# Optimization experiments

Hardware: AMD Instinct MI355X
Metric: run time of the kernel (lower is better)

The kernel has to match this reference:

```python
import jax, jax.numpy as jnp
import numpy as np

B, C, D, H, K = 512, 112, 128, 8, 8  # batch, channels(=seq), d_model, heads, conv kernel
HD = D // H
SCALE = HD ** -0.5
BN_EPS = 1e-5
LN_EPS = 1e-5


def setup_inputs() -> dict:
    key = jax.random.key(0)
    ks = jax.random.split(key, 12)
    s = 0.05
    return {
        "x": jax.random.normal(ks[0], (B, C, D), jnp.float32),
        "conv_w": jax.random.normal(ks[1], (C, 1, K), jnp.float32) * s,
        "conv_b": jax.random.normal(ks[2], (C,), jnp.float32) * s,
        "bn_g": jnp.ones((C,), jnp.float32),
        "bn_b": jnp.zeros((C,), jnp.float32),
        "bn_m": jnp.zeros((C,), jnp.float32),
        "bn_v": jnp.ones((C,), jnp.float32),
        "wq": jax.random.normal(ks[3], (D, D), jnp.float32) * s,
        "bq": jax.random.normal(ks[4], (D,), jnp.float32) * s,
        "wk": jax.random.normal(ks[5], (D, D), jnp.float32) * s,
        "bk": jax.random.normal(ks[6], (D,), jnp.float32) * s,
        "wv": jax.random.normal(ks[7], (D, D), jnp.float32) * s,
        "bv": jax.random.normal(ks[8], (D,), jnp.float32) * s,
        "wo": jax.random.normal(ks[9], (D, D), jnp.float32) * s,
        "bo": jax.random.normal(ks[10], (D,), jnp.float32) * s,
        "ln_g": jnp.ones((D,), jnp.float32),
        "ln_b": jnp.zeros((D,), jnp.float32),
    }


def _forward(x, conv_w, conv_b, bn_g, bn_b, bn_m, bn_v,
             wq, bq, wk, bk, wv, bv, wo, bo, ln_g, ln_b):
    # resnet_1: depthwise Conv1d(padding='same', k=8) -> GELU -> BatchNorm1d (eval)
    # torch 'same' padding for even k: left = (k-1)//2 = 3, right = 4
    h = jax.lax.conv_general_dilated(
        x, conv_w, window_strides=(1,), padding=[(3, 4)],
        dimension_numbers=("NCH", "OIH", "NCH"), feature_group_count=C)
    h = h + conv_b[None, :, None]
    h = jax.nn.gelu(h, approximate=False)
    h = (h - bn_m[None, :, None]) * (bn_g[None, :, None] * jax.lax.rsqrt(bn_v + BN_EPS)[None, :, None]) + bn_b[None, :, None]
    src = x + h  # [B, C, D]; attention treats C as sequence dim

    # multi-head attention (hand-rolled, res_attention path with prev=None)
    q = (src @ wq.T + bq).reshape(B, C, H, HD).transpose(0, 2, 1, 3)  # [B,H,S,hd]
    k = (src @ wk.T + bk).reshape(B, C, H, HD).transpose(0, 2, 1, 3)
    v = (src @ wv.T + bv).reshape(B, C, H, HD).transpose(0, 2, 1, 3)
    scores = jnp.einsum("bhqd,bhkd->bhqk", q, k) * SCALE  # [B,H,S,S]
    attn = jax.nn.softmax(scores, axis=-1)
    out = jnp.einsum("bhqk,bhkd->bhqd", attn, v)  # [B,H,S,hd]
    out = out.transpose(0, 2, 1, 3).reshape(B, C, D)
    out = out @ wo.T + bo

    # residual + LayerNorm over last dim
    src = src + out
    mu = jnp.mean(src, axis=-1, keepdims=True)
    var = jnp.mean(jnp.square(src - mu), axis=-1, keepdims=True)
    src = (src - mu) * jax.lax.rsqrt(var + LN_EPS) * ln_g + ln_b
    return src


def reference(x, conv_w, conv_b, bn_g, bn_b, bn_m, bn_v,
              wq, bq, wk, bk, wv, bv, wo, bo, ln_g, ln_b):
    return _forward(x, conv_w, conv_b, bn_g, bn_b, bn_m, bn_v,
                    wq, bq, wk, bk, wv, bv, wo, bo, ln_g, ln_b)
```

## Files before the change

### kernel.cpp

```cpp
#include <hip/hip_runtime.h>
#include <hip/hip_bf16.h>

#define BB 512
#define CC 112
#define DD 128
#define HH 8
#define HD 16
#define KK 8
#define SROW 140
#define QS 1792

typedef unsigned short u16;
typedef short short8 __attribute__((ext_vector_type(8)));
typedef float f32x4 __attribute__((ext_vector_type(4)));
typedef float f32x16 __attribute__((ext_vector_type(16)));

#define MFMA16(a, b, c) __builtin_amdgcn_mfma_f32_16x16x32_bf16(a, b, c, 0, 0, 0)
#define MFMA32(a, b, c) __builtin_amdgcn_mfma_f32_32x32x16_bf16(a, b, c, 0, 0, 0)

__device__ inline u16 f2bf(float f) {
  union { float f; unsigned u; } v{f};
  unsigned r = (v.u + 0x7FFFu + ((v.u >> 16) & 1u)) >> 16;
  return (u16)r;
}
__device__ inline float bf2f(u16 u) {
  union { unsigned u; float f; } v;
  v.u = ((unsigned)u) << 16;
  return v.f;
}
__device__ inline unsigned pk2(float a, float b) {
  __hip_bfloat162 h = __float22bfloat162_rn(float2{a, b});
  union { __hip_bfloat162 h; unsigned u; } v{h};
  return v.u;
}

__device__ inline unsigned permx32(unsigned x) {
  unsigned a = x, b = x;
  asm("v_permlane32_swap_b32 %0, %1" : "+v"(a), "+v"(b));
  return (threadIdx.x & 32) ? a : b;
}
__device__ inline float permx32f(float x) {
  union { float f; unsigned u; } v{x};
  v.u = permx32(v.u);
  return v.f;
}

__global__ __launch_bounds__(256) void k_wcvt(
    const float* __restrict__ wq, const float* __restrict__ wk,
    const float* __restrict__ wv, const float* __restrict__ wo,
    u16* __restrict__ w_b) {
  const int i = (blockIdx.x * 256 + threadIdx.x);
  const int sel = i >> 12, off = i & 4095;
  const float* w = (sel == 0) ? wq : (sel == 1) ? wk : (sel == 2) ? wv : wo;
  const float4 v = ((const float4*)w)[off];
  ((uint2*)w_b)[i] = uint2{pk2(v.x, v.y), pk2(v.z, v.w)};
}

__global__ __launch_bounds__(1024, 4) void k_fused(
    const float* __restrict__ x, const float* __restrict__ cw,
    const float* __restrict__ cb, const float* __restrict__ bg,
    const float* __restrict__ bb_, const float* __restrict__ bm,
    const float* __restrict__ bv, const u16* __restrict__ w_b,
    const float* __restrict__ bq, const float* __restrict__ bk,
    const float* __restrict__ bvv, const float* __restrict__ bo,
    const float* __restrict__ lg, const float* __restrict__ lb,
    float* __restrict__ out) {
  __shared__ __attribute__((aligned(16))) u16 S[CC * SROW];
  __shared__ __attribute__((aligned(16))) u16 QL[HH * CC * HD];
  __shared__ __attribute__((aligned(16))) u16 KL[HH * CC * HD];
  __shared__ __attribute__((aligned(16))) u16 VTL[HH * HD * CC];
  const int b = blockIdx.x;
  const int t = threadIdx.x;
  const int wave = t >> 6, lane = t & 63;

  const int tg = t >> 3, s = t & 7;
  if (tg < CC) {
    const int row = tg, ch = tg;
    const float4 w0 = *(const float4*)(cw + ch * KK);
    const float4 w1 = *(const float4*)(cw + ch * KK + 4);
    const float cbv = cb[ch];
    const float bscale = bg[ch] * rsqrtf(bv[ch] + 1e-5f);
    const float bmv = bm[ch], bbv = bb_[ch];
    const float* __restrict__ xr = x + ((size_t)b * CC + row) * DD;
    float in[24];
#pragma unroll
    for (int f = 0; f < 6; ++f) {
      const int fi = 4 * s - 1 + f;
      float4 vv = {0.f, 0.f, 0.f, 0.f};
      if (fi >= 0 && fi < 32) vv = ((const float4*)xr)[fi];
      in[f * 4 + 0] = vv.x; in[f * 4 + 1] = vv.y;
      in[f * 4 + 2] = vv.z; in[f * 4 + 3] = vv.w;
    }
    unsigned pkv[8];
#pragma unroll
    for (int i2 = 0; i2 < 8; ++i2) {
      float oo[2];
#pragma unroll
      for (int j = 0; j < 2; ++j) {
        const int i = i2 * 2 + j;
        float a = 0.f;
        a = fmaf(in[i + 1], w0.x, a);
        a = fmaf(in[i + 2], w0.y, a);
        a = fmaf(in[i + 3], w0.z, a);
        a = fmaf(in[i + 4], w0.w, a);
        a = fmaf(in[i + 5], w1.x, a);
        a = fmaf(in[i + 6], w1.y, a);
        a = fmaf(in[i + 7], w1.z, a);
        a = fmaf(in[i + 8], w1.w, a);
        a += cbv;
        const float u = fmaf(0.044715f * a, a, 1.0f);
        const float e = __expf(a * u * -1.5957691216f);
        const float g = a * __frcp_rn(1.f + e);
        oo[j] = in[i + 4] + (g - bmv) * bscale + bbv;
      }
      pkv[i2] = pk2(oo[0], oo[1]);
    }
    u16* srow = S + row * SROW + s * 16;
#pragma unroll
    for (int k2 = 0; k2 < 4; ++k2)
      *(uint2*)(srow + k2 * 4) = ((uint2*)pkv)[k2];
  }
  __syncthreads();

  {
    const int h = wave >> 1, mh = wave & 1;
    const int quad = lane >> 4, n = lane & 15;
    short8 Bf0[4], Bf1[4], Bf2[4];
#pragma unroll
    for (int kf = 0; kf < 4; ++kf) {
      const int wi = (h * 16 + n) * DD + kf * 32 + quad * 8;
      Bf0[kf] = *(const short8*)(w_b + wi);
      Bf1[kf] = *(const short8*)(w_b + 16384 + wi);
      Bf2[kf] = *(const short8*)(w_b + 32768 + wi);
    }
    const float bqv = bq[h * 16 + n];
    const float bkv = bk[h * 16 + n];
    const float bvv2 = bvv[h * 16 + n];
    u16* qlh = QL + h * QS;
    u16* klh = KL + h * QS;
    u16* vlh = VTL + h * QS;
#pragma unroll
    for (int m = 0; m < 4; ++m) {
      const int mt = mh * 4 + m;
      if (mt < 7) {
        short8 A[4];
#pragma unroll
        for (int kf = 0; kf < 4; ++kf)
          A[kf] = *(const short8*)&S[(mt * 16 + n) * SROW + kf * 32 + quad * 8];
        f32x4 aq = {0.f, 0.f, 0.f, 0.f};
        f32x4 ak = {0.f, 0.f, 0.f, 0.f};
        f32x4 av = {0.f, 0.f, 0.f, 0.f};
#pragma unroll
        for (int kf = 0; kf < 4; ++kf) {
          aq = MFMA16(A[kf], Bf0[kf], aq);
          ak = MFMA16(A[kf], Bf1[kf], ak);
          av = MFMA16(A[kf], Bf2[kf], av);
        }
        const int row0 = mt * 16 + quad * 4;
#pragma unroll
        for (int r = 0; r < 4; ++r) {
          qlh[(row0 + r) * HD + n] = f2bf(aq[r] + bqv);
          klh[(row0 + r) * HD + n] = f2bf(ak[r] + bkv);
        }
        *(uint2*)&vlh[n * CC + row0] =
            uint2{pk2(av[0] + bvv2, av[1] + bvv2),
                  pk2(av[2] + bvv2, av[3] + bvv2)};
      }
    }
  }
  __syncthreads();

  {
    const int h = wave >> 1, qh = wave & 1;
    const int lo = lane & 31, hi = lane >> 5, hi8 = hi * 8;
    const u16* qlh = QL + h * QS;
    const u16* klh = KL + h * QS;
    const u16* vlh = VTL + h * QS;
    u16* aoh = QL + h * QS;
    for (int qi = 0; qi < 2; ++qi) {
      const int qt = qh * 2 + qi;
      const int qt0 = qt * 32;
      short8 Bq = {};
      if (qt0 + lo < CC) Bq = *(const short8*)(qlh + (qt0 + lo) * HD + hi8);
      f32x16 sa[4];
#pragma unroll
      for (int mt = 0; mt < 4; ++mt) {
        short8 Ak = {};
        const int key = mt * 32 + lo;
        if (key < CC) Ak = *(const short8*)(klh + key * HD + hi8);
        f32x16 z = {};
        sa[mt] = MFMA32(Ak, Bq, z);
      }
      const float C1 = 0.25f * 1.44269504088896341f;
      float mxp[4] = {-1e30f, -1e30f, -1e30f, -1e30f};
#pragma unroll
      for (int mt = 0; mt < 4; ++mt) {
        const int rmax = (mt == 3) ? 8 : 16;
#pragma unroll
        for (int r = 0; r < 16; ++r)
          if (r < rmax) mxp[r & 3] = fmaxf(mxp[r & 3], sa[mt][r]);
      }
      float mx = fmaxf(fmaxf(mxp[0], mxp[1]), fmaxf(mxp[2], mxp[3]));
      mx = fmaxf(mx, permx32f(mx));
      const float mxc = mx * C1;
      float sp[4] = {0.f, 0.f, 0.f, 0.f};
#pragma unroll
      for (int mt = 0; mt < 4; ++mt) {
        const int rmax = (mt == 3) ? 8 : 16;
#pragma unroll
        for (int r = 0; r < 16; ++r)
          if (r < rmax) {
            const float p = exp2f(fmaf(sa[mt][r], C1, -mxc));
            sa[mt][r] = p;
            sp[r & 3] += p;
          }
      }
      float sum = (sp[0] + sp[1]) + (sp[2] + sp[3]);
      sum += permx32f(sum);
      const float rinv = 1.f / sum;
      unsigned U0[4][4], U1[4][4];
#pragma unroll
      for (int mt = 0; mt < 4; ++mt) {
        const int rqmax = (mt == 3) ? 2 : 4;
#pragma unroll
        for (int rq = 0; rq < 4; ++rq)
          if (rq < rqmax) {
            U0[mt][rq] =
                pk2(sa[mt][4 * rq + 0] * rinv, sa[mt][4 * rq + 1] * rinv);
            U1[mt][rq] =
                pk2(sa[mt][4 * rq + 2] * rinv, sa[mt][4 * rq + 3] * rinv);
          }
      }
      f32x16 oacc = {};
#pragma unroll
      for (int kt = 0; kt < 7; ++kt) {
        const int mt = kt >> 1;
        const int c = 2 * (kt & 1);
        const unsigned own0 = hi ? U0[mt][c + 1] : U0[mt][c];
        const unsigned own1 = hi ? U1[mt][c + 1] : U1[mt][c];
        const unsigned snd0 = hi ? U0[mt][c] : U0[mt][c + 1];
        const unsigned snd1 = hi ? U1[mt][c] : U1[mt][c + 1];
        const unsigned got0 = permx32(snd0);
        const unsigned got1 = permx32(snd1);
        union { unsigned u[4]; short8 s; } ap;
        ap.u[0] = hi ? got0 : own0;
        ap.u[1] = hi ? got1 : own1;
        ap.u[2] = hi ? own0 : got0;
        ap.u[3] = hi ? own1 : got1;
        short8 Bv = {};
        if (lo < HD) Bv = *(const short8*)(vlh + lo * CC + kt * 16 + hi8);
        oacc = MFMA32(ap.s, Bv, oacc);
      }
      if (lo < HD) {
#pragma unroll
        for (int r = 0; r < 16; ++r) {
          const int rr = (r & 3) + 8 * (r >> 2) + 4 * hi;
          if (qt0 + rr < CC) aoh[(qt0 + rr) * HD + lo] = f2bf(oacc[r]);
        }
      }
    }
  }
  __syncthreads();

  if (wave < 7) {
    const int quad = lane >> 4, n = lane & 15;
    const int mt = wave;
    const u16* __restrict__ w_bo = w_b + 3 * 16384;
    short8 A[4];
#pragma unroll
    for (int kf = 0; kf < 4; ++kf) {
      const int head = 2 * kf + (quad >> 1);
      A[kf] = *(const short8*)&QL[head * QS + (mt * 16 + n) * HD + (quad & 1) * 8];
    }
    float v[8][4];
#pragma unroll
    for (int nt = 0; nt < 8; ++nt) {
      f32x4 acc = {0.f, 0.f, 0.f, 0.f};
#pragma unroll
      for (int kf = 0; kf < 4; ++kf) {
        const short8 Bf =
            *(const short8*)(w_bo + (nt * 16 + n) * DD + kf * 32 + quad * 8);
        acc = MFMA16(A[kf], Bf, acc);
      }
      const int col = nt * 16 + n;
      const float bcol = bo[col];
#pragma unroll
      for (int r = 0; r < 4; ++r)
        v[nt][r] = acc[r] + bcol +
                   bf2f(S[(mt * 16 + quad * 4 + r) * SROW + col]);
    }
    float sum[4] = {0.f, 0.f, 0.f, 0.f}, sq[4] = {0.f, 0.f, 0.f, 0.f};
#pragma unroll
    for (int nt = 0; nt < 8; ++nt)
#pragma unroll
      for (int r = 0; r < 4; ++r) {
        sum[r] += v[nt][r];
        sq[r] = fmaf(v[nt][r], v[nt][r], sq[r]);
      }
#pragma unroll
    for (int d = 1; d < 16; d <<= 1)
#pragma unroll
      for (int r = 0; r < 4; ++r) {
        sum[r] += __shfl_xor(sum[r], d);
        sq[r] += __shfl_xor(sq[r], d);
      }
    float mu[4], rs[4];
#pragma unroll
    for (int r = 0; r < 4; ++r) {
      mu[r] = sum[r] * (1.f / DD);
      const float var = sq[r] * (1.f / DD) - mu[r] * mu[r];
      rs[r] = rsqrtf(var + 1e-5f);
    }
#pragma unroll
    for (int nt = 0; nt < 8; ++nt) {
      const int col = nt * 16 + n;
      const float g = lg[col], be = lb[col];
#pragma unroll
      for (int r = 0; r < 4; ++r)
        out[((size_t)b * CC + mt * 16 + quad * 4 + r) * DD + col] =
            (v[nt][r] - mu[r]) * rs[r] * g + be;
    }
  }
}

extern "C" void kernel_launch(void* const* d_in, const int* in_sizes, int n_in,
                              void* d_out, int out_size, void* d_ws,
                              size_t ws_size, hipStream_t stream) {
  (void)in_sizes; (void)n_in; (void)out_size; (void)ws_size;
  const float* x   = (const float*)d_in[0];
  const float* cw  = (const float*)d_in[1];
  const float* cb  = (const float*)d_in[2];
  const float* bg  = (const float*)d_in[3];
  const float* bb  = (const float*)d_in[4];
  const float* bm  = (const float*)d_in[5];
  const float* bv  = (const float*)d_in[6];
  const float* wq  = (const float*)d_in[7];
  const float* bq  = (const float*)d_in[8];
  const float* wk  = (const float*)d_in[9];
  const float* bk  = (const float*)d_in[10];
  const float* wv  = (const float*)d_in[11];
  const float* bvv = (const float*)d_in[12];
  const float* wo  = (const float*)d_in[13];
  const float* bo  = (const float*)d_in[14];
  const float* lg  = (const float*)d_in[15];
  const float* lb  = (const float*)d_in[16];
  float* out = (float*)d_out;

  u16* w_b = (u16*)d_ws;

  k_wcvt<<<64, 256, 0, stream>>>(wq, wk, wv, wo, w_b);
  k_fused<<<BB, 1024, 0, stream>>>(x, cw, cb, bg, bb, bm, bv, w_b, bq, bk,
                                   bvv, bo, lg, lb, out);
}
```

Before: 173.3 us.

## Split fused kernel into conv and attention kernels with register-resident V

```diff
diff --git a/kernel.cpp b/kernel.cpp
--- a/kernel.cpp
+++ b/kernel.cpp
@@ -7,7 +7,6 @@
 #define HH 8
 #define HD 16
 #define KK 8
-#define SROW 140
 #define QS 1792
 
 typedef unsigned short u16;
@@ -45,35 +44,17 @@
   return v.f;
 }
 
-__global__ __launch_bounds__(256) void k_wcvt(
-    const float* __restrict__ wq, const float* __restrict__ wk,
-    const float* __restrict__ wv, const float* __restrict__ wo,
-    u16* __restrict__ w_b) {
-  const int i = (blockIdx.x * 256 + threadIdx.x);
-  const int sel = i >> 12, off = i & 4095;
-  const float* w = (sel == 0) ? wq : (sel == 1) ? wk : (sel == 2) ? wv : wo;
-  const float4 v = ((const float4*)w)[off];
-  ((uint2*)w_b)[i] = uint2{pk2(v.x, v.y), pk2(v.z, v.w)};
-}
-
-__global__ __launch_bounds__(1024, 4) void k_fused(
+__global__ __launch_bounds__(512, 4) void k_conv(
     const float* __restrict__ x, const float* __restrict__ cw,
     const float* __restrict__ cb, const float* __restrict__ bg,
     const float* __restrict__ bb_, const float* __restrict__ bm,
-    const float* __restrict__ bv, const u16* __restrict__ w_b,
-    const float* __restrict__ bq, const float* __restrict__ bk,
-    const float* __restrict__ bvv, const float* __restrict__ bo,
-    const float* __restrict__ lg, const float* __restrict__ lb,
-    float* __restrict__ out) {
-  __shared__ __attribute__((aligned(16))) u16 S[CC * SROW];
-  __shared__ __attribute__((aligned(16))) u16 QL[HH * CC * HD];
-  __shared__ __attribute__((aligned(16))) u16 KL[HH * CC * HD];
-  __shared__ __attribute__((aligned(16))) u16 VTL[HH * HD * CC];
+    const float* __restrict__ bv, const float* __restrict__ wq,
+    const float* __restrict__ wk, const float* __restrict__ wv,
+    const float* __restrict__ wo, u16* __restrict__ src_b,
+    u16* __restrict__ w_b) {
   const int b = blockIdx.x;
   const int t = threadIdx.x;
-  const int wave = t >> 6, lane = t & 63;
-
-  const int tg = t >> 3, s = t & 7;
+  const int tg = t >> 2, sub = t & 3;
   if (tg < CC) {
     const int row = tg, ch = tg;
     const float4 w0 = *(const float4*)(cw + ch * KK);
@@ -82,18 +63,18 @@
     const float bscale = bg[ch] * rsqrtf(bv[ch] + 1e-5f);
     const float bmv = bm[ch], bbv = bb_[ch];
     const float* __restrict__ xr = x + ((size_t)b * CC + row) * DD;
-    float in[24];
-#pragma unroll
-    for (int f = 0; f < 6; ++f) {
-      const int fi = 4 * s - 1 + f;
+    float in[40];
+#pragma unroll
+    for (int f = 0; f < 10; ++f) {
+      const int fi = 8 * sub - 1 + f;
       float4 vv = {0.f, 0.f, 0.f, 0.f};
       if (fi >= 0 && fi < 32) vv = ((const float4*)xr)[fi];
       in[f * 4 + 0] = vv.x; in[f * 4 + 1] = vv.y;
       in[f * 4 + 2] = vv.z; in[f * 4 + 3] = vv.w;
     }
-    unsigned pkv[8];
-#pragma unroll
-    for (int i2 = 0; i2 < 8; ++i2) {
+    unsigned pkv[16];
+#pragma unroll
+    for (int i2 = 0; i2 < 16; ++i2) {
       float oo[2];
 #pragma unroll
       for (int j = 0; j < 2; ++j) {
@@ -110,78 +91,87 @@
         a += cbv;
         const float u = fmaf(0.044715f * a, a, 1.0f);
         const float e = __expf(a * u * -1.5957691216f);
-        const float g = a * __frcp_rn(1.f + e);
-        oo[j] = in[i + 4] + (g - bmv) * bscale + bbv;
+        const float g2 = a * __frcp_rn(1.f + e);
+        oo[j] = in[i + 4] + (g2 - bmv) * bscale + bbv;
       }
       pkv[i2] = pk2(oo[0], oo[1]);
     }
-    u16* srow = S + row * SROW + s * 16;
-#pragma unroll
-    for (int k2 = 0; k2 < 4; ++k2)
-      *(uint2*)(srow + k2 * 4) = ((uint2*)pkv)[k2];
+    uint4* gsr = (uint4*)(src_b + ((size_t)b * CC + row) * DD + sub * 32);
+#pragma unroll
+    for (int k4 = 0; k4 < 4; ++k4) gsr[k4] = ((uint4*)pkv)[k4];
+  } else if (t >= 448) {
+    const int p = b * 64 + (t - 448);
+    const int sel = p >> 13, off = p & 8191;
+    const float* w = (sel == 0) ? wq : (sel == 1) ? wk : (sel == 2) ? wv : wo;
+    const float2 v = ((const float2*)w)[off];
+    ((unsigned*)w_b)[p] = pk2(v.x, v.y);
   }
-  __syncthreads();
-
+}
+
+__global__ __launch_bounds__(512, 4) void k_main(
+    const u16* __restrict__ src_b, const u16* __restrict__ w_b,
+    const float* __restrict__ bq, const float* __restrict__ bk,
+    const float* __restrict__ bvv, const float* __restrict__ bo,
+    const float* __restrict__ lg, const float* __restrict__ lb,
+    float* __restrict__ out) {
+  __shared__ __attribute__((aligned(16))) u16 QO[HH * CC * HD];
+  __shared__ __attribute__((aligned(16))) u16 KL[HH * CC * HD];
+  const int b = blockIdx.x;
+  const int t = threadIdx.x;
+  const int wave = t >> 6, lane = t & 63;
+  const int h = wave;
+  const int quad = lane >> 4, n = lane & 15;
+
+  unsigned pv[14];
   {
-    const int h = wave >> 1, mh = wave & 1;
-    const int quad = lane >> 4, n = lane & 15;
-    short8 Bf0[4], Bf1[4], Bf2[4];
+    short8 Wq[4], Wk[4], Wv[4];
 #pragma unroll
     for (int kf = 0; kf < 4; ++kf) {
       const int wi = (h * 16 + n) * DD + kf * 32 + quad * 8;
-      Bf0[kf] = *(const short8*)(w_b + wi);
-      Bf1[kf] = *(const short8*)(w_b + 16384 + wi);
-      Bf2[kf] = *(const short8*)(w_b + 32768 + wi);
+      Wq[kf] = *(const short8*)(w_b + wi);
+      Wk[kf] = *(const short8*)(w_b + 16384 + wi);
+      Wv[kf] = *(const short8*)(w_b + 32768 + wi);
     }
     const float bqv = bq[h * 16 + n];
     const float bkv = bk[h * 16 + n];
     const float bvv2 = bvv[h * 16 + n];
-    u16* qlh = QL + h * QS;
+    u16* qoh = QO + h * QS;
     u16* klh = KL + h * QS;
-    u16* vlh = VTL + h * QS;
-#pragma unroll
-    for (int m = 0; m < 4; ++m) {
-      const int mt = mh * 4 + m;
-      if (mt < 7) {
-        short8 A[4];
-#pragma unroll
-        for (int kf = 0; kf < 4; ++kf)
-          A[kf] = *(const short8*)&S[(mt * 16 + n) * SROW + kf * 32 + quad * 8];
-        f32x4 aq = {0.f, 0.f, 0.f, 0.f};
-        f32x4 ak = {0.f, 0.f, 0.f, 0.f};
-        f32x4 av = {0.f, 0.f, 0.f, 0.f};
-#pragma unroll
-        for (int kf = 0; kf < 4; ++kf) {
-          aq = MFMA16(A[kf], Bf0[kf], aq);
-          ak = MFMA16(A[kf], Bf1[kf], ak);
-          av = MFMA16(A[kf], Bf2[kf], av);
-        }
-        const int row0 = mt * 16 + quad * 4;
-#pragma unroll
-        for (int r = 0; r < 4; ++r) {
-          qlh[(row0 + r) * HD + n] = f2bf(aq[r] + bqv);
-          klh[(row0 + r) * HD + n] = f2bf(ak[r] + bkv);
-        }
-        *(uint2*)&vlh[n * CC + row0] =
-            uint2{pk2(av[0] + bvv2, av[1] + bvv2),
-                  pk2(av[2] + bvv2, av[3] + bvv2)};
-      }
+    const u16* __restrict__ sp = src_b + (size_t)b * CC * DD;
+#pragma unroll
+    for (int mt = 0; mt < 7; ++mt) {
+      short8 A[4];
+#pragma unroll
+      for (int kf = 0; kf < 4; ++kf)
+        A[kf] = *(const short8*)(sp + (mt * 16 + n) * DD + kf * 32 + quad * 8);
+      f32x4 aq = {0.f, 0.f, 0.f, 0.f};
+      f32x4 ak = {0.f, 0.f, 0.f, 0.f};
+      f32x4 av = {0.f, 0.f, 0.f, 0.f};
+#pragma unroll
+      for (int kf = 0; kf < 4; ++kf) {
+        aq = MFMA16(A[kf], Wq[kf], aq);
+        ak = MFMA16(A[kf], Wk[kf], ak);
+        av = MFMA16(A[kf], Wv[kf], av);
+      }
+      const int row0 = mt * 16 + quad * 4;
+#pragma unroll
+      for (int r = 0; r < 4; ++r) {
+        qoh[(row0 + r) * HD + n] = f2bf(aq[r] + bqv);
+        klh[(row0 + r) * HD + n] = f2bf(ak[r] + bkv);
+      }
+      pv[2 * mt] = pk2(av[0] + bvv2, av[1] + bvv2);
+      pv[2 * mt + 1] = pk2(av[2] + bvv2, av[3] + bvv2);
     }
   }
-  __syncthreads();
 
   {
-    const int h = wave >> 1, qh = wave & 1;
     const int lo = lane & 31, hi = lane >> 5, hi8 = hi * 8;
-    const u16* qlh = QL + h * QS;
+    u16* qoh = QO + h * QS;
     const u16* klh = KL + h * QS;
-    const u16* vlh = VTL + h * QS;
-    u16* aoh = QL + h * QS;
-    for (int qi = 0; qi < 2; ++qi) {
-      const int qt = qh * 2 + qi;
+    for (int qt = 0; qt < 4; ++qt) {
       const int qt0 = qt * 32;
       short8 Bq = {};
-      if (qt0 + lo < CC) Bq = *(const short8*)(qlh + (qt0 + lo) * HD + hi8);
+      if (qt0 + lo < CC) Bq = *(const short8*)(qoh + (qt0 + lo) * HD + hi8);
       f32x16 sa[4];
 #pragma unroll
       for (int mt = 0; mt < 4; ++mt) {
@@ -203,7 +193,7 @@
       float mx = fmaxf(fmaxf(mxp[0], mxp[1]), fmaxf(mxp[2], mxp[3]));
       mx = fmaxf(mx, permx32f(mx));
       const float mxc = mx * C1;
-      float sp[4] = {0.f, 0.f, 0.f, 0.f};
+      float sp4[4] = {0.f, 0.f, 0.f, 0.f};
 #pragma unroll
       for (int mt = 0; mt < 4; ++mt) {
         const int rmax = (mt == 3) ? 8 : 16;
@@ -212,10 +202,10 @@
           if (r < rmax) {
             const float p = exp2f(fmaf(sa[mt][r], C1, -mxc));
             sa[mt][r] = p;
-            sp[r & 3] += p;
+            sp4[r & 3] += p;
           }
       }
-      float sum = (sp[0] + sp[1]) + (sp[2] + sp[3]);
+      float sum = (sp4[0] + sp4[1]) + (sp4[2] + sp4[3]);
       sum += permx32f(sum);
       const float rinv = 1.f / sum;
       unsigned U0[4][4], U1[4][4];
@@ -247,15 +237,18 @@
         ap.u[1] = hi ? got1 : own1;
         ap.u[2] = hi ? own0 : got0;
         ap.u[3] = hi ? own1 : got1;
-        short8 Bv = {};
-        if (lo < HD) Bv = *(const short8*)(vlh + lo * CC + kt * 16 + hi8);
-        oacc = MFMA32(ap.s, Bv, oacc);
+        union { unsigned u[4]; short8 s; } bvf;
+        bvf.u[0] = pv[2 * kt];
+        bvf.u[1] = pv[2 * kt + 1];
+        bvf.u[2] = __shfl_xor(pv[2 * kt], 16);
+        bvf.u[3] = __shfl_xor(pv[2 * kt + 1], 16);
+        oacc = MFMA32(ap.s, bvf.s, oacc);
       }
       if (lo < HD) {
 #pragma unroll
         for (int r = 0; r < 16; ++r) {
           const int rr = (r & 3) + 8 * (r >> 2) + 4 * hi;
-          if (qt0 + rr < CC) aoh[(qt0 + rr) * HD + lo] = f2bf(oacc[r]);
+          if (qt0 + rr < CC) qoh[(qt0 + rr) * HD + lo] = f2bf(oacc[r]);
         }
       }
     }
@@ -263,14 +256,14 @@
   __syncthreads();
 
   if (wave < 7) {
-    const int quad = lane >> 4, n = lane & 15;
     const int mt = wave;
     const u16* __restrict__ w_bo = w_b + 3 * 16384;
     short8 A[4];
 #pragma unroll
     for (int kf = 0; kf < 4; ++kf) {
       const int head = 2 * kf + (quad >> 1);
-      A[kf] = *(const short8*)&QL[head * QS + (mt * 16 + n) * HD + (quad & 1) * 8];
+      A[kf] =
+          *(const short8*)&QO[head * QS + (mt * 16 + n) * HD + (quad & 1) * 8];
     }
     float v[8][4];
 #pragma unroll
@@ -286,8 +279,9 @@
       const float bcol = bo[col];
 #pragma unroll
       for (int r = 0; r < 4; ++r)
-        v[nt][r] = acc[r] + bcol +
-                   bf2f(S[(mt * 16 + quad * 4 + r) * SROW + col]);
+        v[nt][r] =
+            acc[r] + bcol +
+            bf2f(src_b[((size_t)b * CC + mt * 16 + quad * 4 + r) * DD + col]);
     }
     float sum[4] = {0.f, 0.f, 0.f, 0.f}, sq[4] = {0.f, 0.f, 0.f, 0.f};
 #pragma unroll
@@ -346,9 +340,12 @@
   const float* lb  = (const float*)d_in[16];
   float* out = (float*)d_out;
 
-  u16* w_b = (u16*)d_ws;
-
-  k_wcvt<<<64, 256, 0, stream>>>(wq, wk, wv, wo, w_b);
-  k_fused<<<BB, 1024, 0, stream>>>(x, cw, cb, bg, bb, bm, bv, w_b, bq, bk,
-                                   bvv, bo, lg, lb, out);
-}
+  const size_t NE = (size_t)BB * CC * DD;
+  u16* ub = (u16*)d_ws;
+  u16* src_b = ub;
+  u16* w_b   = ub + NE;
+
+  k_conv<<<BB, 512, 0, stream>>>(x, cw, cb, bg, bb, bm, bv, wq, wk, wv, wo,
+                                 src_b, w_b);
+  k_main<<<BB, 512, 0, stream>>>(src_b, w_b, bq, bk, bvv, bo, lg, lb, out);
+}
```

After: 169.2 us. 2.3% less time.
